# Optimization experiments

Measured on AMD Instinct MI355X. Metric: run time of the kernel, lower is better.

## Reference

```python
import jax, jax.numpy as jnp
import numpy as np

N_NODES = 20000
N_EDGES = 320000
IN_CH = 512
HEADS = 4
OUT_CH = 128
NEG_SLOPE = 0.2  # PyG GATConv default leaky_relu slope


def setup_inputs() -> dict:
    key = jax.random.key(0)
    k1, k2, k3, k4, k5 = jax.random.split(key, 5)
    x = jax.random.normal(k1, (N_NODES, IN_CH), dtype=jnp.float32)
    edge_index = jax.random.randint(k2, (2, N_EDGES), 0, N_NODES, dtype=jnp.int64)
    # Learned parameters (glorot-ish scaling)
    W = jax.random.normal(k3, (IN_CH, HEADS * OUT_CH), dtype=jnp.float32) * np.float32(1.0 / np.sqrt(IN_CH))
    att_src = jax.random.normal(k4, (HEADS, OUT_CH), dtype=jnp.float32) * np.float32(0.1)
    att_dst = jax.random.normal(k5, (HEADS, OUT_CH), dtype=jnp.float32) * np.float32(0.1)
    bias = jnp.zeros((OUT_CH,), dtype=jnp.float32)
    return {"x": x, "W": W, "att_src": att_src, "att_dst": att_dst, "bias": bias, "edge_index": edge_index}


def reference(x, W, att_src, att_dst, bias, edge_index):
    N = x.shape[0]
    H, C = att_src.shape
    # add self-loops (PyG GATConv default add_self_loops=True)
    loop = jnp.arange(N, dtype=edge_index.dtype)
    ei = jnp.concatenate([edge_index, jnp.stack([loop, loop])], axis=1)
    src, dst = ei[0], ei[1]
    # linear projection: [N, H, C]
    xl = (x @ W).reshape(N, H, C)
    # per-node attention halves: [N, H]
    a_s = jnp.einsum('nhc,hc->nh', xl, att_src)
    a_d = jnp.einsum('nhc,hc->nh', xl, att_dst)
    # per-edge logits + segment softmax over incoming edges (grouped by dst)
    alpha = jax.nn.leaky_relu(a_s[src] + a_d[dst], negative_slope=NEG_SLOPE)  # [E, H]
    amax = jax.ops.segment_max(alpha, dst, num_segments=N)  # every node has a self-loop -> no empty segments
    ae = jnp.exp(alpha - amax[dst])
    denom = jax.ops.segment_sum(ae, dst, num_segments=N)
    alpha = ae / (denom[dst] + 1e-16)
    # weighted scatter-add of source features: [N, H, C]
    out = jax.ops.segment_sum(alpha[:, :, None] * xl[src], dst, num_segments=N)
    # concat=False -> mean over heads, then bias [C]
    out = out.mean(axis=1) + bias
    return jax.nn.elu(out)
```

## Files before the change

### kernel.cpp

```cpp
#include <hip/hip_runtime.h>
#include <math.h>

#define N_NODES 20000
#define N_PAD 20096
#define N_EDGES 320000
#define IN_CH 512
#define HEADS 4
#define OUT_CH 128
#define HC 512
#define NEG_SLOPE 0.2f

#define CVX_BLOCKS 5024
#define CVW_BLOCKS 64
#define CNT_BLOCKS 1250
#define ATT_BLOCKS 1250

typedef __attribute__((ext_vector_type(8))) short short8;
typedef __attribute__((ext_vector_type(4))) float float4v;

__device__ __forceinline__ int detect_is64(const int* __restrict__ ei32) {
    int is64 = 1;
    #pragma unroll
    for (int i = 0; i < 32; i++) is64 &= (ei32[2 * i + 1] == 0);
    return is64;
}

__device__ __forceinline__ int edge_at(const void* ei, int is64, long long idx) {
    return is64 ? (int)((const long long*)ei)[idx] : ((const int*)ei)[idx];
}

__device__ __forceinline__ unsigned short f2bf(float f) {
    union { float f; unsigned u; } v; v.f = f;
    unsigned r = v.u + 0x7fffu + ((v.u >> 16) & 1u);
    return (unsigned short)(r >> 16);
}

__device__ __forceinline__ void bf8_decode(uint4 r, float* f) {
    f[0] = __uint_as_float(r.x << 16); f[1] = __uint_as_float(r.x & 0xffff0000u);
    f[2] = __uint_as_float(r.y << 16); f[3] = __uint_as_float(r.y & 0xffff0000u);
    f[4] = __uint_as_float(r.z << 16); f[5] = __uint_as_float(r.z & 0xffff0000u);
    f[6] = __uint_as_float(r.w << 16); f[7] = __uint_as_float(r.w & 0xffff0000u);
}

__device__ __forceinline__ float leaky(float t) { return t > 0.f ? t : NEG_SLOPE * t; }

__device__ __forceinline__ float sel_head(float4 w, int hd) {
    float lo = (hd & 1) ? w.y : w.x;
    float hi = (hd & 1) ? w.w : w.z;
    return (hd & 2) ? hi : lo;
}

__global__ __launch_bounds__(256) void fusedA_kernel(const float* __restrict__ x,
                                                     const float* __restrict__ W,
                                                     unsigned short* __restrict__ xb,
                                                     unsigned short* __restrict__ Wt,
                                                     const void* __restrict__ ei,
                                                     int* __restrict__ counts) {
    __shared__ float tile[64][65];
    int b = blockIdx.x;
    if (b < CVX_BLOCKS) {
        size_t i = ((size_t)b * 256 + threadIdx.x) * 8;
        unsigned short o[8];
        if (i < (size_t)N_NODES * IN_CH) {
            float4 f0 = *(const float4*)&x[i];
            float4 f1 = *(const float4*)&x[i + 4];
            o[0] = f2bf(f0.x); o[1] = f2bf(f0.y); o[2] = f2bf(f0.z); o[3] = f2bf(f0.w);
            o[4] = f2bf(f1.x); o[5] = f2bf(f1.y); o[6] = f2bf(f1.z); o[7] = f2bf(f1.w);
        } else {
            for (int k = 0; k < 8; k++) o[k] = 0;
        }
        *(short8*)&xb[i] = *(short8*)o;
    } else if (b < CVX_BLOCKS + CVW_BLOCKS) {
        int idx = b - CVX_BLOCKS;
        int k0 = (idx & 7) * 64, n0 = (idx >> 3) * 64;
        int t = threadIdx.x, r = t >> 6, c = t & 63;
        for (int rr = r; rr < 64; rr += 4)
            tile[rr][c] = W[(size_t)(k0 + rr) * HC + n0 + c];
        __syncthreads();
        for (int rr = r; rr < 64; rr += 4)
            Wt[(size_t)(n0 + rr) * IN_CH + k0 + c] = f2bf(tile[c][rr]);
    } else {
        int is64 = detect_is64((const int*)ei);
        int e = (b - CVX_BLOCKS - CVW_BLOCKS) * 256 + threadIdx.x;
        if (e < N_EDGES) {
            int dst = edge_at(ei, is64, (long long)N_EDGES + e);
            atomicAdd(&counts[dst], 1);
        }
    }
}

__global__ __launch_bounds__(256) void gemm_kernel(const unsigned short* __restrict__ A,
                                                   const unsigned short* __restrict__ Bt,
                                                   unsigned short* __restrict__ Cb) {
    __shared__ __align__(16) unsigned short As[128 * 32];
    __shared__ __align__(16) unsigned short Bs[128 * 32];
    const int bm = blockIdx.y * 128;
    const int bn = blockIdx.x * 128;
    const int t = threadIdx.x;
    const int wv = t >> 6, lane = t & 63;
    const int wm = wv & 1, wn = wv >> 1;
    const int lm = lane & 15, lk = lane >> 4;

    float4v acc[4][4];
    #pragma unroll
    for (int i = 0; i < 4; i++)
        #pragma unroll
        for (int j = 0; j < 4; j++) acc[i][j] = (float4v){0.f, 0.f, 0.f, 0.f};

    const int srow = t >> 2;
    const int skof = (t & 3) * 8;

    for (int k0 = 0; k0 < IN_CH; k0 += 32) {
        __syncthreads();
        #pragma unroll
        for (int q = 0; q < 2; q++) {
            const unsigned short* gA = A + (size_t)(bm + q * 64 + srow) * IN_CH + k0 + skof;
            const unsigned short* gB = Bt + (size_t)(bn + q * 64 + srow) * IN_CH + k0 + skof;
            __builtin_amdgcn_global_load_lds((const __attribute__((address_space(1))) void*)gA,
                                             (__attribute__((address_space(3))) void*)&As[q * 2048 + t * 8], 16, 0, 0);
            __builtin_amdgcn_global_load_lds((const __attribute__((address_space(1))) void*)gB,
                                             (__attribute__((address_space(3))) void*)&Bs[q * 2048 + t * 8], 16, 0, 0);
        }
        __syncthreads();

        short8 af[4], bf[4];
        #pragma unroll
        for (int i = 0; i < 4; i++)
            af[i] = *(const short8*)&As[(wm * 64 + i * 16 + lm) * 32 + lk * 8];
        #pragma unroll
        for (int j = 0; j < 4; j++)
            bf[j] = *(const short8*)&Bs[(wn * 64 + j * 16 + lm) * 32 + lk * 8];
        #pragma unroll
        for (int i = 0; i < 4; i++)
            #pragma unroll
            for (int j = 0; j < 4; j++)
                acc[i][j] = __builtin_amdgcn_mfma_f32_16x16x32_bf16(af[i], bf[j], acc[i][j], 0, 0, 0);
    }

    #pragma unroll
    for (int i = 0; i < 4; i++) {
        #pragma unroll
        for (int r = 0; r < 4; r++) {
            int row = bm + wm * 64 + i * 16 + lk * 4 + r;
            if (row < N_NODES) {
                #pragma unroll
                for (int j = 0; j < 4; j++) {
                    int col = bn + wn * 64 + j * 16 + lm;
                    Cb[(size_t)row * HC + col] = f2bf(acc[i][j][r]);
                }
            }
        }
    }
}

__global__ __launch_bounds__(1024) void scanattn_kernel(const int* __restrict__ counts,
                                                        int* __restrict__ offsets,
                                                        const unsigned short* __restrict__ xlb,
                                                        const float* __restrict__ att_s,
                                                        const float* __restrict__ att_d,
                                                        float* __restrict__ a_s,
                                                        float* __restrict__ a_d) {
    int b = blockIdx.x;
    if (b == 0) {
        const int CHUNK = 20;
        int tid = threadIdx.x;
        int base = tid * CHUNK;
        int c[CHUNK];
        #pragma unroll
        for (int k = 0; k < CHUNK; k++) {
            int i = base + k;
            c[k] = (i < N_NODES) ? counts[i] : 0;
        }
        int pre[CHUNK];
        int sum = 0;
        #pragma unroll
        for (int k = 0; k < CHUNK; k++) { pre[k] = sum; sum += c[k]; }

        int lane = tid & 63, wvv = tid >> 6;
        int s = sum;
        #pragma unroll
        for (int off = 1; off < 64; off <<= 1) {
            int u = __shfl_up(s, off, 64);
            if (lane >= off) s += u;
        }
        __shared__ int wsum[16];
        if (lane == 63) wsum[wvv] = s;
        __syncthreads();
        if (tid < 16) {
            int u = wsum[tid];
            #pragma unroll
            for (int off = 1; off < 16; off <<= 1) {
                int w = __shfl_up(u, off, 64);
                if (tid >= off) u += w;
            }
            wsum[tid] = u;
        }
        __syncthreads();
        int wbase = (wvv == 0) ? 0 : wsum[wvv - 1];
        int excl = wbase + s - sum;
        #pragma unroll
        for (int k = 0; k < CHUNK; k++) {
            int i = base + k;
            if (i < N_NODES) offsets[i] = excl + pre[k];
        }
        if (tid == 1023) offsets[N_NODES] = wbase + s;
    } else {
        int node = (b - 1) * 16 + (threadIdx.x >> 6);
        if (node >= N_NODES) return;
        int lane = threadIdx.x & 63;
        int hd = lane >> 4;
        uint4 r = *(const uint4*)&xlb[(size_t)node * HC + lane * 8];
        float f[8];
        bf8_decode(r, f);
        float4 s0 = *(const float4*)&att_s[lane * 8];
        float4 s1 = *(const float4*)&att_s[lane * 8 + 4];
        float4 d0 = *(const float4*)&att_d[lane * 8];
        float4 d1 = *(const float4*)&att_d[lane * 8 + 4];
        float s = f[0]*s0.x + f[1]*s0.y + f[2]*s0.z + f[3]*s0.w
                + f[4]*s1.x + f[5]*s1.y + f[6]*s1.z + f[7]*s1.w;
        float d = f[0]*d0.x + f[1]*d0.y + f[2]*d0.z + f[3]*d0.w
                + f[4]*d1.x + f[5]*d1.y + f[6]*d1.z + f[7]*d1.w;
        #pragma unroll
        for (int off = 1; off < 16; off <<= 1) {
            s += __shfl_xor(s, off, 64);
            d += __shfl_xor(d, off, 64);
        }
        if ((lane & 15) == 0) {
            a_s[node * 4 + hd] = s;
            a_d[node * 4 + hd] = d;
        }
    }
}

__global__ __launch_bounds__(256) void scatterw_kernel(const void* __restrict__ ei,
                                                       const int* __restrict__ offsets,
                                                       int* __restrict__ cursor,
                                                       int* __restrict__ sorted_src,
                                                       const float* __restrict__ a_s,
                                                       const float* __restrict__ a_d,
                                                       float* __restrict__ edge_w) {
    int is64 = detect_is64((const int*)ei);
    int e = blockIdx.x * 256 + threadIdx.x;
    if (e < N_EDGES) {
        int dst = edge_at(ei, is64, (long long)N_EDGES + e);
        int src = edge_at(ei, is64, e);
        int pos = offsets[dst] + atomicAdd(&cursor[dst], 1);
        sorted_src[pos] = src;
        float4 as4 = *(const float4*)&a_s[src * 4];
        float4 ad4 = *(const float4*)&a_d[dst * 4];
        float4 w;
        w.x = __expf(leaky(as4.x + ad4.x));
        w.y = __expf(leaky(as4.y + ad4.y));
        w.z = __expf(leaky(as4.z + ad4.z));
        w.w = __expf(leaky(as4.w + ad4.w));
        *(float4*)&edge_w[(size_t)pos * 4] = w;
    }
}

__global__ __launch_bounds__(256) void gather_kernel(const unsigned short* __restrict__ xlb,
                                                     const float* __restrict__ a_s,
                                                     const float* __restrict__ a_d,
                                                     const int* __restrict__ offsets,
                                                     const int* __restrict__ sorted_src,
                                                     const float* __restrict__ edge_w,
                                                     const float* __restrict__ bias,
                                                     float* __restrict__ out) {
    __shared__ float cl[2][64][9];
    int wv = threadIdx.x >> 6;
    int nib = wv >> 1;
    int sub = wv & 1;
    int node = blockIdx.x * 2 + nib;
    int lane = threadIdx.x & 63;
    int hd = lane >> 4;
    int beg = offsets[node], end = offsets[node + 1];

    const unsigned short* xrow = xlb + lane * 8;
    float acc[8] = {0, 0, 0, 0, 0, 0, 0, 0};
    float denom = 0.f;

    if (sub == 0) {
        float4 as4 = *(const float4*)&a_s[node * 4];
        float4 ad4 = *(const float4*)&a_d[node * 4];
        float4 ws;
        ws.x = __expf(leaky(as4.x + ad4.x));
        ws.y = __expf(leaky(as4.y + ad4.y));
        ws.z = __expf(leaky(as4.z + ad4.z));
        ws.w = __expf(leaky(as4.w + ad4.w));
        float w = sel_head(ws, hd);
        denom = w;
        uint4 r = *(const uint4*)(xrow + (size_t)node * HC);
        float f[8];
        bf8_decode(r, f);
        #pragma unroll
        for (int k = 0; k < 8; k++) acc[k] = w * f[k];
    }

    for (int c0 = beg + sub * 4; c0 < end; c0 += 8) {
        int n = end - c0;
        if (n >= 4) {
            int s0 = sorted_src[c0];
            int s1 = sorted_src[c0 + 1];
            int s2 = sorted_src[c0 + 2];
            int s3 = sorted_src[c0 + 3];
            uint4 r0 = *(const uint4*)(xrow + (size_t)s0 * HC);
            uint4 r1 = *(const uint4*)(xrow + (size_t)s1 * HC);
            uint4 r2 = *(const uint4*)(xrow + (size_t)s2 * HC);
            uint4 r3 = *(const uint4*)(xrow + (size_t)s3 * HC);
            float4 wa = *(const float4*)&edge_w[(size_t)c0 * 4];
            float4 wb = *(const float4*)&edge_w[(size_t)(c0 + 1) * 4];
            float4 wc = *(const float4*)&edge_w[(size_t)(c0 + 2) * 4];
            float4 wd = *(const float4*)&edge_w[(size_t)(c0 + 3) * 4];
            float w0 = sel_head(wa, hd), w1 = sel_head(wb, hd);
            float w2 = sel_head(wc, hd), w3 = sel_head(wd, hd);
            denom += (w0 + w1) + (w2 + w3);
            float f0[8], f1[8], f2[8], f3[8];
            bf8_decode(r0, f0);
            bf8_decode(r1, f1);
            bf8_decode(r2, f2);
            bf8_decode(r3, f3);
            #pragma unroll
            for (int k = 0; k < 8; k++)
                acc[k] += (w0 * f0[k] + w1 * f1[k]) + (w2 * f2[k] + w3 * f3[k]);
        } else {
            for (int j = 0; j < n; j++) {
                int s0 = sorted_src[c0 + j];
                uint4 r0 = *(const uint4*)(xrow + (size_t)s0 * HC);
                float4 wa = *(const float4*)&edge_w[(size_t)(c0 + j) * 4];
                float w0 = sel_head(wa, hd);
                denom += w0;
                float f0[8];
                bf8_decode(r0, f0);
                #pragma unroll
                for (int k = 0; k < 8; k++) acc[k] += w0 * f0[k];
            }
        }
    }

    if (sub == 1) {
        #pragma unroll
        for (int k = 0; k < 8; k++) cl[nib][lane][k] = acc[k];
        cl[nib][lane][8] = denom;
    }
    __syncthreads();
    if (sub == 0) {
        #pragma unroll
        for (int k = 0; k < 8; k++) acc[k] += cl[nib][lane][k];
        denom += cl[nib][lane][8];

        float rd = 0.25f / (denom + 1e-16f);
        float v[8];
        #pragma unroll
        for (int k = 0; k < 8; k++) {
            float t = acc[k] * rd;
            t += __shfl_xor(t, 16, 64);
            t += __shfl_xor(t, 32, 64);
            v[k] = t;
        }
        if (hd == 0) {
            float4 b0 = *(const float4*)&bias[lane * 8];
            float4 b1 = *(const float4*)&bias[lane * 8 + 4];
            float o[8];
            o[0] = v[0] + b0.x; o[1] = v[1] + b0.y; o[2] = v[2] + b0.z; o[3] = v[3] + b0.w;
            o[4] = v[4] + b1.x; o[5] = v[5] + b1.y; o[6] = v[6] + b1.z; o[7] = v[7] + b1.w;
            #pragma unroll
            for (int k = 0; k < 8; k++) o[k] = o[k] > 0.f ? o[k] : expm1f(o[k]);
            *(float4*)&out[(size_t)node * OUT_CH + lane * 8]     = make_float4(o[0], o[1], o[2], o[3]);
            *(float4*)&out[(size_t)node * OUT_CH + lane * 8 + 4] = make_float4(o[4], o[5], o[6], o[7]);
        }
    }
}

extern "C" void kernel_launch(void* const* d_in, const int* in_sizes, int n_in,
                              void* d_out, int out_size, void* d_ws, size_t ws_size,
                              hipStream_t stream) {
    const float* x       = (const float*)d_in[0];
    const float* W       = (const float*)d_in[1];
    const float* att_src = (const float*)d_in[2];
    const float* att_dst = (const float*)d_in[3];
    const float* bias    = (const float*)d_in[4];
    const void*  ei      = d_in[5];
    float* out = (float*)d_out;

    char* ws = (char*)d_ws;
    size_t off = 0;
    unsigned short* xlb = (unsigned short*)(ws + off); off += (size_t)N_PAD * HC * sizeof(unsigned short);
    float* a_s     = (float*)(ws + off); off += (size_t)N_NODES * HEADS * sizeof(float);
    float* a_d     = (float*)(ws + off); off += (size_t)N_NODES * HEADS * sizeof(float);
    int* counts    = (int*)(ws + off);   off += (size_t)N_NODES * sizeof(int);
    int* cursor    = (int*)(ws + off);   off += (size_t)N_NODES * sizeof(int);
    int* offsets   = (int*)(ws + off);   off += (size_t)(N_NODES + 1) * sizeof(int);
    off = (off + 15) & ~(size_t)15;
    int* sorted_src = (int*)(ws + off);  off += (size_t)N_EDGES * sizeof(int);
    off = (off + 15) & ~(size_t)15;
    float* edge_w  = (float*)(ws + off); off += (size_t)N_EDGES * HEADS * sizeof(float);
    unsigned short* xb = (unsigned short*)(ws + off); off += (size_t)N_PAD * IN_CH * sizeof(unsigned short);
    unsigned short* Wt = (unsigned short*)(ws + off); off += (size_t)IN_CH * HC * sizeof(unsigned short);

    hipMemsetAsync(counts, 0, 2u * N_NODES * sizeof(int), stream);
    fusedA_kernel<<<CVX_BLOCKS + CVW_BLOCKS + CNT_BLOCKS, 256, 0, stream>>>(x, W, xb, Wt, ei, counts);
    gemm_kernel<<<dim3(HC / 128, N_PAD / 128), 256, 0, stream>>>(xb, Wt, xlb);
    scanattn_kernel<<<1 + ATT_BLOCKS, 1024, 0, stream>>>(counts, offsets, xlb, att_src, att_dst, a_s, a_d);
    scatterw_kernel<<<(N_EDGES + 255) / 256, 256, 0, stream>>>(ei, offsets, cursor, sorted_src, a_s, a_d, edge_w);
    gather_kernel<<<N_NODES / 2, 256, 0, stream>>>(xlb, a_s, a_d, offsets, sorted_src, edge_w, bias, out);
}
```

Measured before the change: 215.8 us.

## Store projected features channel-group-major and gather per group with recomputed edge weights

The GEMM output is rewritten into 8 channel-group slabs of [N_PAD][64] (4 heads x 16 channels), so each gather block works on one slab whose footprint fits better in cache. The gather kernel now handles one node per wave, with 8 edge slots per wave and shuffle reductions instead of LDS. Edge weights are recomputed from a_s/a_d inside the gather instead of being precomputed and stored as edge_w in the scatter kernel. This drops the edge_w write and read, at the cost of 8x redundant reads of sorted_src, a_s and exp per edge, and launches 8x more blocks.

```diff
diff --git a/kernel.cpp b/kernel.cpp
--- a/kernel.cpp
+++ b/kernel.cpp
@@ -18,6 +18,7 @@
 typedef __attribute__((ext_vector_type(8))) short short8;
 typedef __attribute__((ext_vector_type(4))) float float4v;
 
+
 __device__ __forceinline__ int detect_is64(const int* __restrict__ ei32) {
     int is64 = 1;
     #pragma unroll
@@ -43,12 +44,6 @@
 }
 
 __device__ __forceinline__ float leaky(float t) { return t > 0.f ? t : NEG_SLOPE * t; }
-
-__device__ __forceinline__ float sel_head(float4 w, int hd) {
-    float lo = (hd & 1) ? w.y : w.x;
-    float hi = (hd & 1) ? w.w : w.z;
-    return (hd & 2) ? hi : lo;
-}
 
 __global__ __launch_bounds__(256) void fusedA_kernel(const float* __restrict__ x,
                                                      const float* __restrict__ W,
@@ -137,6 +132,7 @@
                 acc[i][j] = __builtin_amdgcn_mfma_f32_16x16x32_bf16(af[i], bf[j], acc[i][j], 0, 0, 0);
     }
 
+    const int h = bn >> 7;
     #pragma unroll
     for (int i = 0; i < 4; i++) {
         #pragma unroll
@@ -145,8 +141,8 @@
             if (row < N_NODES) {
                 #pragma unroll
                 for (int j = 0; j < 4; j++) {
-                    int col = bn + wn * 64 + j * 16 + lm;
-                    Cb[(size_t)row * HC + col] = f2bf(acc[i][j][r]);
+                    int g = wn * 4 + j;
+                    Cb[((size_t)g * N_PAD + row) * 64 + h * 16 + lm] = f2bf(acc[i][j][r]);
                 }
             }
         }
@@ -209,7 +205,8 @@
         if (node >= N_NODES) return;
         int lane = threadIdx.x & 63;
         int hd = lane >> 4;
-        uint4 r = *(const uint4*)&xlb[(size_t)node * HC + lane * 8];
+        int g2 = (lane & 15) >> 1;
+        uint4 r = *(const uint4*)&xlb[((size_t)g2 * N_PAD + node) * 64 + hd * 16 + (lane & 1) * 8];
         float f[8];
         bf8_decode(r, f);
         float4 s0 = *(const float4*)&att_s[lane * 8];
@@ -235,10 +232,7 @@
 __global__ __launch_bounds__(256) void scatterw_kernel(const void* __restrict__ ei,
                                                        const int* __restrict__ offsets,
                                                        int* __restrict__ cursor,
-                                                       int* __restrict__ sorted_src,
-                                                       const float* __restrict__ a_s,
-                                                       const float* __restrict__ a_d,
-                                                       float* __restrict__ edge_w) {
+                                                       int* __restrict__ sorted_src) {
     int is64 = detect_is64((const int*)ei);
     int e = blockIdx.x * 256 + threadIdx.x;
     if (e < N_EDGES) {
@@ -246,14 +240,6 @@
         int src = edge_at(ei, is64, e);
         int pos = offsets[dst] + atomicAdd(&cursor[dst], 1);
         sorted_src[pos] = src;
-        float4 as4 = *(const float4*)&a_s[src * 4];
-        float4 ad4 = *(const float4*)&a_d[dst * 4];
-        float4 w;
-        w.x = __expf(leaky(as4.x + ad4.x));
-        w.y = __expf(leaky(as4.y + ad4.y));
-        w.z = __expf(leaky(as4.z + ad4.z));
-        w.w = __expf(leaky(as4.w + ad4.w));
-        *(float4*)&edge_w[(size_t)pos * 4] = w;
     }
 }
 
@@ -262,111 +248,73 @@
                                                      const float* __restrict__ a_d,
                                                      const int* __restrict__ offsets,
                                                      const int* __restrict__ sorted_src,
-                                                     const float* __restrict__ edge_w,
                                                      const float* __restrict__ bias,
                                                      float* __restrict__ out) {
-    __shared__ float cl[2][64][9];
-    int wv = threadIdx.x >> 6;
-    int nib = wv >> 1;
-    int sub = wv & 1;
-    int node = blockIdx.x * 2 + nib;
+    int g    = blockIdx.x & 7;
+    int q    = blockIdx.x >> 3;
+    int wv   = threadIdx.x >> 6;
+    int node = q * 4 + wv;
     int lane = threadIdx.x & 63;
-    int hd = lane >> 4;
+    int slot = lane >> 3;
+    int sub  = lane & 7;
+    int h    = sub >> 1;
+    int cp   = sub & 1;
+
+    const unsigned short* xg = xlb + ((size_t)g * N_PAD) * 64 + h * 16 + cp * 8;
+    float ad = a_d[node * 4 + h];
     int beg = offsets[node], end = offsets[node + 1];
 
-    const unsigned short* xrow = xlb + lane * 8;
     float acc[8] = {0, 0, 0, 0, 0, 0, 0, 0};
     float denom = 0.f;
 
-    if (sub == 0) {
-        float4 as4 = *(const float4*)&a_s[node * 4];
-        float4 ad4 = *(const float4*)&a_d[node * 4];
-        float4 ws;
-        ws.x = __expf(leaky(as4.x + ad4.x));
-        ws.y = __expf(leaky(as4.y + ad4.y));
-        ws.z = __expf(leaky(as4.z + ad4.z));
-        ws.w = __expf(leaky(as4.w + ad4.w));
-        float w = sel_head(ws, hd);
+    if (slot == 0) {
+        float w = __expf(leaky(a_s[node * 4 + h] + ad));
         denom = w;
-        uint4 r = *(const uint4*)(xrow + (size_t)node * HC);
+        uint4 r = *(const uint4*)(xg + (size_t)node * 64);
         float f[8];
         bf8_decode(r, f);
         #pragma unroll
         for (int k = 0; k < 8; k++) acc[k] = w * f[k];
     }
 
-    for (int c0 = beg + sub * 4; c0 < end; c0 += 8) {
-        int n = end - c0;
-        if (n >= 4) {
-            int s0 = sorted_src[c0];
-            int s1 = sorted_src[c0 + 1];
-            int s2 = sorted_src[c0 + 2];
-            int s3 = sorted_src[c0 + 3];
-            uint4 r0 = *(const uint4*)(xrow + (size_t)s0 * HC);
-            uint4 r1 = *(const uint4*)(xrow + (size_t)s1 * HC);
-            uint4 r2 = *(const uint4*)(xrow + (size_t)s2 * HC);
-            uint4 r3 = *(const uint4*)(xrow + (size_t)s3 * HC);
-            float4 wa = *(const float4*)&edge_w[(size_t)c0 * 4];
-            float4 wb = *(const float4*)&edge_w[(size_t)(c0 + 1) * 4];
-            float4 wc = *(const float4*)&edge_w[(size_t)(c0 + 2) * 4];
-            float4 wd = *(const float4*)&edge_w[(size_t)(c0 + 3) * 4];
-            float w0 = sel_head(wa, hd), w1 = sel_head(wb, hd);
-            float w2 = sel_head(wc, hd), w3 = sel_head(wd, hd);
-            denom += (w0 + w1) + (w2 + w3);
-            float f0[8], f1[8], f2[8], f3[8];
-            bf8_decode(r0, f0);
-            bf8_decode(r1, f1);
-            bf8_decode(r2, f2);
-            bf8_decode(r3, f3);
-            #pragma unroll
-            for (int k = 0; k < 8; k++)
-                acc[k] += (w0 * f0[k] + w1 * f1[k]) + (w2 * f2[k] + w3 * f3[k]);
-        } else {
-            for (int j = 0; j < n; j++) {
-                int s0 = sorted_src[c0 + j];
-                uint4 r0 = *(const uint4*)(xrow + (size_t)s0 * HC);
-                float4 wa = *(const float4*)&edge_w[(size_t)(c0 + j) * 4];
-                float w0 = sel_head(wa, hd);
-                denom += w0;
-                float f0[8];
-                bf8_decode(r0, f0);
-                #pragma unroll
-                for (int k = 0; k < 8; k++) acc[k] += w0 * f0[k];
-            }
-        }
-    }
-
-    if (sub == 1) {
-        #pragma unroll
-        for (int k = 0; k < 8; k++) cl[nib][lane][k] = acc[k];
-        cl[nib][lane][8] = denom;
-    }
-    __syncthreads();
-    if (sub == 0) {
-        #pragma unroll
-        for (int k = 0; k < 8; k++) acc[k] += cl[nib][lane][k];
-        denom += cl[nib][lane][8];
-
-        float rd = 0.25f / (denom + 1e-16f);
-        float v[8];
+    for (int e = beg + slot; e < end; e += 8) {
+        int s = sorted_src[e];
+        float w = __expf(leaky(a_s[s * 4 + h] + ad));
+        uint4 r = *(const uint4*)(xg + (size_t)s * 64);
+        denom += w;
+        float f[8];
+        bf8_decode(r, f);
+        #pragma unroll
+        for (int k = 0; k < 8; k++) acc[k] += w * f[k];
+    }
+
+    #pragma unroll
+    for (int off = 8; off < 64; off <<= 1) {
+        denom += __shfl_xor(denom, off, 64);
+        #pragma unroll
+        for (int k = 0; k < 8; k++) acc[k] += __shfl_xor(acc[k], off, 64);
+    }
+
+    float rd = 0.25f / (denom + 1e-16f);
+    float v[8];
+    #pragma unroll
+    for (int k = 0; k < 8; k++) {
+        float t = acc[k] * rd;
+        t += __shfl_xor(t, 2, 64);
+        t += __shfl_xor(t, 4, 64);
+        v[k] = t;
+    }
+
+    if (lane < 2) {
+        int cbase = g * 16 + cp * 8;
+        float o[8];
         #pragma unroll
         for (int k = 0; k < 8; k++) {
-            float t = acc[k] * rd;
-            t += __shfl_xor(t, 16, 64);
-            t += __shfl_xor(t, 32, 64);
-            v[k] = t;
-        }
-        if (hd == 0) {
-            float4 b0 = *(const float4*)&bias[lane * 8];
-            float4 b1 = *(const float4*)&bias[lane * 8 + 4];
-            float o[8];
-            o[0] = v[0] + b0.x; o[1] = v[1] + b0.y; o[2] = v[2] + b0.z; o[3] = v[3] + b0.w;
-            o[4] = v[4] + b1.x; o[5] = v[5] + b1.y; o[6] = v[6] + b1.z; o[7] = v[7] + b1.w;
-            #pragma unroll
-            for (int k = 0; k < 8; k++) o[k] = o[k] > 0.f ? o[k] : expm1f(o[k]);
-            *(float4*)&out[(size_t)node * OUT_CH + lane * 8]     = make_float4(o[0], o[1], o[2], o[3]);
-            *(float4*)&out[(size_t)node * OUT_CH + lane * 8 + 4] = make_float4(o[4], o[5], o[6], o[7]);
-        }
+            float t = v[k] + bias[cbase + k];
+            o[k] = t > 0.f ? t : expm1f(t);
+        }
+        *(float4*)&out[(size_t)node * OUT_CH + cbase]     = make_float4(o[0], o[1], o[2], o[3]);
+        *(float4*)&out[(size_t)node * OUT_CH + cbase + 4] = make_float4(o[4], o[5], o[6], o[7]);
     }
 }
 
@@ -392,7 +340,6 @@
     off = (off + 15) & ~(size_t)15;
     int* sorted_src = (int*)(ws + off);  off += (size_t)N_EDGES * sizeof(int);
     off = (off + 15) & ~(size_t)15;
-    float* edge_w  = (float*)(ws + off); off += (size_t)N_EDGES * HEADS * sizeof(float);
     unsigned short* xb = (unsigned short*)(ws + off); off += (size_t)N_PAD * IN_CH * sizeof(unsigned short);
     unsigned short* Wt = (unsigned short*)(ws + off); off += (size_t)IN_CH * HC * sizeof(unsigned short);
 
@@ -400,6 +347,6 @@
     fusedA_kernel<<<CVX_BLOCKS + CVW_BLOCKS + CNT_BLOCKS, 256, 0, stream>>>(x, W, xb, Wt, ei, counts);
     gemm_kernel<<<dim3(HC / 128, N_PAD / 128), 256, 0, stream>>>(xb, Wt, xlb);
     scanattn_kernel<<<1 + ATT_BLOCKS, 1024, 0, stream>>>(counts, offsets, xlb, att_src, att_dst, a_s, a_d);
-    scatterw_kernel<<<(N_EDGES + 255) / 256, 256, 0, stream>>>(ei, offsets, cursor, sorted_src, a_s, a_d, edge_w);
-    gather_kernel<<<N_NODES / 2, 256, 0, stream>>>(xlb, a_s, a_d, offsets, sorted_src, edge_w, bias, out);
-}
+    scatterw_kernel<<<(N_EDGES + 255) / 256, 256, 0, stream>>>(ei, offsets, cursor, sorted_src);
+    gather_kernel<<<(N_NODES / 4) * 8, 256, 0, stream>>>(xlb, a_s, a_d, offsets, sorted_src, bias, out);
+}
```

After: 272.8 us. 1.26x slower.

## Fuse attention dot products into GEMM epilogue, reuse count-atomic positions, widen gather

Applied to the files above, without the earlier changes.

The per-node attention halves a_s/a_d are now computed in the GEMM epilogue from fp32 accumulators using shuffle and shared-memory reductions, so the separate pass that re-read the bf16 projection is gone. The edge counting pass saves each edge's atomic return value as its slot within its destination segment, which removes the second atomic cursor pass in scatter. The gather kernel now gives each node a full block of four waves that split the edges and reduce through shared memory. The costs are a heavier GEMM epilogue with an extra barrier, a new per-edge position buffer to write and read, and twice as many gather blocks.

```diff
diff --git a/kernel.cpp b/kernel.cpp
--- a/kernel.cpp
+++ b/kernel.cpp
@@ -13,7 +13,6 @@
 #define CVX_BLOCKS 5024
 #define CVW_BLOCKS 64
 #define CNT_BLOCKS 1250
-#define ATT_BLOCKS 1250
 
 typedef __attribute__((ext_vector_type(8))) short short8;
 typedef __attribute__((ext_vector_type(4))) float float4v;
@@ -55,7 +54,8 @@
                                                      unsigned short* __restrict__ xb,
                                                      unsigned short* __restrict__ Wt,
                                                      const void* __restrict__ ei,
-                                                     int* __restrict__ counts) {
+                                                     int* __restrict__ counts,
+                                                     int* __restrict__ epos) {
     __shared__ float tile[64][65];
     int b = blockIdx.x;
     if (b < CVX_BLOCKS) {
@@ -84,16 +84,23 @@
         int e = (b - CVX_BLOCKS - CVW_BLOCKS) * 256 + threadIdx.x;
         if (e < N_EDGES) {
             int dst = edge_at(ei, is64, (long long)N_EDGES + e);
-            atomicAdd(&counts[dst], 1);
+            int p = atomicAdd(&counts[dst], 1);
+            epos[e] = p;
         }
     }
 }
 
 __global__ __launch_bounds__(256) void gemm_kernel(const unsigned short* __restrict__ A,
                                                    const unsigned short* __restrict__ Bt,
-                                                   unsigned short* __restrict__ Cb) {
+                                                   unsigned short* __restrict__ Cb,
+                                                   const float* __restrict__ att_s,
+                                                   const float* __restrict__ att_d,
+                                                   float* __restrict__ a_s,
+                                                   float* __restrict__ a_d) {
     __shared__ __align__(16) unsigned short As[128 * 32];
     __shared__ __align__(16) unsigned short Bs[128 * 32];
+    __shared__ float ssum[128][2];
+    __shared__ float dsum[128][2];
     const int bm = blockIdx.y * 128;
     const int bn = blockIdx.x * 128;
     const int t = threadIdx.x;
@@ -151,90 +158,104 @@
             }
         }
     }
-}
-
-__global__ __launch_bounds__(1024) void scanattn_kernel(const int* __restrict__ counts,
-                                                        int* __restrict__ offsets,
-                                                        const unsigned short* __restrict__ xlb,
-                                                        const float* __restrict__ att_s,
-                                                        const float* __restrict__ att_d,
-                                                        float* __restrict__ a_s,
-                                                        float* __restrict__ a_d) {
-    int b = blockIdx.x;
-    if (b == 0) {
-        const int CHUNK = 20;
-        int tid = threadIdx.x;
-        int base = tid * CHUNK;
-        int c[CHUNK];
-        #pragma unroll
-        for (int k = 0; k < CHUNK; k++) {
-            int i = base + k;
-            c[k] = (i < N_NODES) ? counts[i] : 0;
-        }
-        int pre[CHUNK];
-        int sum = 0;
-        #pragma unroll
-        for (int k = 0; k < CHUNK; k++) { pre[k] = sum; sum += c[k]; }
-
-        int lane = tid & 63, wvv = tid >> 6;
-        int s = sum;
-        #pragma unroll
-        for (int off = 1; off < 64; off <<= 1) {
-            int u = __shfl_up(s, off, 64);
-            if (lane >= off) s += u;
-        }
-        __shared__ int wsum[16];
-        if (lane == 63) wsum[wvv] = s;
-        __syncthreads();
-        if (tid < 16) {
-            int u = wsum[tid];
-            #pragma unroll
-            for (int off = 1; off < 16; off <<= 1) {
-                int w = __shfl_up(u, off, 64);
-                if (tid >= off) u += w;
+
+    const int h = bn >> 7;
+    float as_w[4], ad_w[4];
+    #pragma unroll
+    for (int j = 0; j < 4; j++) {
+        int col = bn + wn * 64 + j * 16 + lm;
+        as_w[j] = att_s[col];
+        ad_w[j] = att_d[col];
+    }
+    float ps[4][4], pd[4][4];
+    #pragma unroll
+    for (int i = 0; i < 4; i++)
+        #pragma unroll
+        for (int r = 0; r < 4; r++) {
+            float s = 0.f, d = 0.f;
+            #pragma unroll
+            for (int j = 0; j < 4; j++) { s += acc[i][j][r] * as_w[j]; d += acc[i][j][r] * ad_w[j]; }
+            ps[i][r] = s; pd[i][r] = d;
+        }
+    #pragma unroll
+    for (int off = 1; off < 16; off <<= 1) {
+        #pragma unroll
+        for (int i = 0; i < 4; i++)
+            #pragma unroll
+            for (int r = 0; r < 4; r++) {
+                ps[i][r] += __shfl_xor(ps[i][r], off, 64);
+                pd[i][r] += __shfl_xor(pd[i][r], off, 64);
             }
-            wsum[tid] = u;
-        }
-        __syncthreads();
-        int wbase = (wvv == 0) ? 0 : wsum[wvv - 1];
-        int excl = wbase + s - sum;
-        #pragma unroll
-        for (int k = 0; k < CHUNK; k++) {
-            int i = base + k;
-            if (i < N_NODES) offsets[i] = excl + pre[k];
-        }
-        if (tid == 1023) offsets[N_NODES] = wbase + s;
-    } else {
-        int node = (b - 1) * 16 + (threadIdx.x >> 6);
-        if (node >= N_NODES) return;
-        int lane = threadIdx.x & 63;
-        int hd = lane >> 4;
-        uint4 r = *(const uint4*)&xlb[(size_t)node * HC + lane * 8];
-        float f[8];
-        bf8_decode(r, f);
-        float4 s0 = *(const float4*)&att_s[lane * 8];
-        float4 s1 = *(const float4*)&att_s[lane * 8 + 4];
-        float4 d0 = *(const float4*)&att_d[lane * 8];
-        float4 d1 = *(const float4*)&att_d[lane * 8 + 4];
-        float s = f[0]*s0.x + f[1]*s0.y + f[2]*s0.z + f[3]*s0.w
-                + f[4]*s1.x + f[5]*s1.y + f[6]*s1.z + f[7]*s1.w;
-        float d = f[0]*d0.x + f[1]*d0.y + f[2]*d0.z + f[3]*d0.w
-                + f[4]*d1.x + f[5]*d1.y + f[6]*d1.z + f[7]*d1.w;
+    }
+    if (lm == 0) {
+        #pragma unroll
+        for (int i = 0; i < 4; i++)
+            #pragma unroll
+            for (int r = 0; r < 4; r++) {
+                int rl = wm * 64 + i * 16 + lk * 4 + r;
+                ssum[rl][wn] = ps[i][r];
+                dsum[rl][wn] = pd[i][r];
+            }
+    }
+    __syncthreads();
+    if (t < 128) {
+        int row = bm + t;
+        if (row < N_NODES) {
+            a_s[row * 4 + h] = ssum[t][0] + ssum[t][1];
+            a_d[row * 4 + h] = dsum[t][0] + dsum[t][1];
+        }
+    }
+}
+
+__global__ __launch_bounds__(1024) void scan_kernel(const int* __restrict__ counts,
+                                                    int* __restrict__ offsets) {
+    const int CHUNK = 20;
+    int tid = threadIdx.x;
+    int base = tid * CHUNK;
+    int c[CHUNK];
+    #pragma unroll
+    for (int k = 0; k < CHUNK; k++) {
+        int i = base + k;
+        c[k] = (i < N_NODES) ? counts[i] : 0;
+    }
+    int pre[CHUNK];
+    int sum = 0;
+    #pragma unroll
+    for (int k = 0; k < CHUNK; k++) { pre[k] = sum; sum += c[k]; }
+
+    int lane = tid & 63, wvv = tid >> 6;
+    int s = sum;
+    #pragma unroll
+    for (int off = 1; off < 64; off <<= 1) {
+        int u = __shfl_up(s, off, 64);
+        if (lane >= off) s += u;
+    }
+    __shared__ int wsum[16];
+    if (lane == 63) wsum[wvv] = s;
+    __syncthreads();
+    if (tid < 16) {
+        int u = wsum[tid];
         #pragma unroll
         for (int off = 1; off < 16; off <<= 1) {
-            s += __shfl_xor(s, off, 64);
-            d += __shfl_xor(d, off, 64);
-        }
-        if ((lane & 15) == 0) {
-            a_s[node * 4 + hd] = s;
-            a_d[node * 4 + hd] = d;
-        }
-    }
+            int w = __shfl_up(u, off, 64);
+            if (tid >= off) u += w;
+        }
+        wsum[tid] = u;
+    }
+    __syncthreads();
+    int wbase = (wvv == 0) ? 0 : wsum[wvv - 1];
+    int excl = wbase + s - sum;
+    #pragma unroll
+    for (int k = 0; k < CHUNK; k++) {
+        int i = base + k;
+        if (i < N_NODES) offsets[i] = excl + pre[k];
+    }
+    if (tid == 1023) offsets[N_NODES] = wbase + s;
 }
 
 __global__ __launch_bounds__(256) void scatterw_kernel(const void* __restrict__ ei,
                                                        const int* __restrict__ offsets,
-                                                       int* __restrict__ cursor,
+                                                       const int* __restrict__ epos,
                                                        int* __restrict__ sorted_src,
                                                        const float* __restrict__ a_s,
                                                        const float* __restrict__ a_d,
@@ -244,7 +265,7 @@
     if (e < N_EDGES) {
         int dst = edge_at(ei, is64, (long long)N_EDGES + e);
         int src = edge_at(ei, is64, e);
-        int pos = offsets[dst] + atomicAdd(&cursor[dst], 1);
+        int pos = offsets[dst] + epos[e];
         sorted_src[pos] = src;
         float4 as4 = *(const float4*)&a_s[src * 4];
         float4 ad4 = *(const float4*)&a_d[dst * 4];
@@ -265,11 +286,9 @@
                                                      const float* __restrict__ edge_w,
                                                      const float* __restrict__ bias,
                                                      float* __restrict__ out) {
-    __shared__ float cl[2][64][9];
-    int wv = threadIdx.x >> 6;
-    int nib = wv >> 1;
-    int sub = wv & 1;
-    int node = blockIdx.x * 2 + nib;
+    __shared__ float cl[3][64][9];
+    int sub = threadIdx.x >> 6;
+    int node = blockIdx.x;
     int lane = threadIdx.x & 63;
     int hd = lane >> 4;
     int beg = offsets[node], end = offsets[node + 1];
@@ -295,7 +314,7 @@
         for (int k = 0; k < 8; k++) acc[k] = w * f[k];
     }
 
-    for (int c0 = beg + sub * 4; c0 < end; c0 += 8) {
+    for (int c0 = beg + sub * 4; c0 < end; c0 += 16) {
         int n = end - c0;
         if (n >= 4) {
             int s0 = sorted_src[c0];
@@ -336,16 +355,19 @@
         }
     }
 
-    if (sub == 1) {
-        #pragma unroll
-        for (int k = 0; k < 8; k++) cl[nib][lane][k] = acc[k];
-        cl[nib][lane][8] = denom;
+    if (sub != 0) {
+        #pragma unroll
+        for (int k = 0; k < 8; k++) cl[sub - 1][lane][k] = acc[k];
+        cl[sub - 1][lane][8] = denom;
     }
     __syncthreads();
     if (sub == 0) {
         #pragma unroll
-        for (int k = 0; k < 8; k++) acc[k] += cl[nib][lane][k];
-        denom += cl[nib][lane][8];
+        for (int p = 0; p < 3; p++) {
+            #pragma unroll
+            for (int k = 0; k < 8; k++) acc[k] += cl[p][lane][k];
+            denom += cl[p][lane][8];
+        }
 
         float rd = 0.25f / (denom + 1e-16f);
         float v[8];
@@ -387,19 +409,19 @@
     float* a_s     = (float*)(ws + off); off += (size_t)N_NODES * HEADS * sizeof(float);
     float* a_d     = (float*)(ws + off); off += (size_t)N_NODES * HEADS * sizeof(float);
     int* counts    = (int*)(ws + off);   off += (size_t)N_NODES * sizeof(int);
-    int* cursor    = (int*)(ws + off);   off += (size_t)N_NODES * sizeof(int);
     int* offsets   = (int*)(ws + off);   off += (size_t)(N_NODES + 1) * sizeof(int);
     off = (off + 15) & ~(size_t)15;
+    int* epos      = (int*)(ws + off);   off += (size_t)N_EDGES * sizeof(int);
     int* sorted_src = (int*)(ws + off);  off += (size_t)N_EDGES * sizeof(int);
     off = (off + 15) & ~(size_t)15;
     float* edge_w  = (float*)(ws + off); off += (size_t)N_EDGES * HEADS * sizeof(float);
     unsigned short* xb = (unsigned short*)(ws + off); off += (size_t)N_PAD * IN_CH * sizeof(unsigned short);
     unsigned short* Wt = (unsigned short*)(ws + off); off += (size_t)IN_CH * HC * sizeof(unsigned short);
 
-    hipMemsetAsync(counts, 0, 2u * N_NODES * sizeof(int), stream);
-    fusedA_kernel<<<CVX_BLOCKS + CVW_BLOCKS + CNT_BLOCKS, 256, 0, stream>>>(x, W, xb, Wt, ei, counts);
-    gemm_kernel<<<dim3(HC / 128, N_PAD / 128), 256, 0, stream>>>(xb, Wt, xlb);
-    scanattn_kernel<<<1 + ATT_BLOCKS, 1024, 0, stream>>>(counts, offsets, xlb, att_src, att_dst, a_s, a_d);
-    scatterw_kernel<<<(N_EDGES + 255) / 256, 256, 0, stream>>>(ei, offsets, cursor, sorted_src, a_s, a_d, edge_w);
-    gather_kernel<<<N_NODES / 2, 256, 0, stream>>>(xlb, a_s, a_d, offsets, sorted_src, edge_w, bias, out);
-}
+    hipMemsetAsync(counts, 0, N_NODES * sizeof(int), stream);
+    fusedA_kernel<<<CVX_BLOCKS + CVW_BLOCKS + CNT_BLOCKS, 256, 0, stream>>>(x, W, xb, Wt, ei, counts, epos);
+    gemm_kernel<<<dim3(HC / 128, N_PAD / 128), 256, 0, stream>>>(xb, Wt, xlb, att_src, att_dst, a_s, a_d);
+    scan_kernel<<<1, 1024, 0, stream>>>(counts, offsets);
+    scatterw_kernel<<<(N_EDGES + 255) / 256, 256, 0, stream>>>(ei, offsets, epos, sorted_src, a_s, a_d, edge_w);
+    gather_kernel<<<N_NODES, 256, 0, stream>>>(xlb, a_s, a_d, offsets, sorted_src, edge_w, bias, out);
+}
```

Result: slower. 220.2 us (+2.0%).
